# Kernel tuning notes

Hardware: AMD Instinct MI355X
Metric: run time of the kernel (lower is better)

Reference implementation:

```python
import jax, jax.numpy as jnp
import numpy as np

DEPTH = 3
HIDDEN = 300
ATOM_FDIM = 133
BOND_FDIM = 147


def setup_inputs() -> dict:
    key = jax.random.key(0)
    ks = jax.random.split(key, 10)
    n_atoms, n_bonds, max_nb, n_mols = 200000, 400000, 6, 10000
    f_atoms = jax.random.normal(ks[0], (n_atoms, ATOM_FDIM), dtype=jnp.float32)
    f_bonds = jax.random.normal(ks[1], (n_bonds, BOND_FDIM), dtype=jnp.float32)
    a2b = jax.random.randint(ks[2], (n_atoms, max_nb), 0, n_bonds)
    b2a = jax.random.randint(ks[3], (n_bonds,), 0, n_atoms)
    b2revb = jax.random.randint(ks[4], (n_bonds,), 0, n_bonds)
    # learned parameters (fan-in scaled)
    W_i = jax.random.normal(ks[5], (BOND_FDIM, HIDDEN), dtype=jnp.float32) / np.sqrt(BOND_FDIM)
    W_h = jax.random.normal(ks[6], (HIDDEN, HIDDEN), dtype=jnp.float32) / np.sqrt(HIDDEN)
    W_o = jax.random.normal(ks[7], (ATOM_FDIM + HIDDEN, HIDDEN), dtype=jnp.float32) / np.sqrt(ATOM_FDIM + HIDDEN)
    b_o = jnp.zeros((HIDDEN,), dtype=jnp.float32)
    return {"f_atoms": f_atoms, "f_bonds": f_bonds, "a2b": a2b, "b2a": b2a,
            "b2revb": b2revb, "W_i": W_i, "W_h": W_h, "W_o": W_o, "b_o": b_o,
            "n_mols": n_mols}


def reference(f_atoms, f_bonds, a2b, b2a, b2revb, W_i, W_h, W_o, b_o, n_mols):
    act = jax.nn.relu
    # input = W_i(f_bonds); message = act(input)
    inp = f_bonds @ W_i                       # [n_bonds, H]
    message = act(inp)
    for _ in range(DEPTH - 1):
        nei_a_message = message[a2b]          # [n_atoms, max_nb, H] gather
        a_message = nei_a_message.sum(axis=1)  # [n_atoms, H]
        rev_message = message[b2revb]         # [n_bonds, H]
        message = a_message[b2a] - rev_message
        message = act(inp + message @ W_h)
    # final atom readout
    a_message = message[a2b].sum(axis=1)      # [n_atoms, H]
    a_input = jnp.concatenate([f_atoms, a_message], axis=1)
    atom_hiddens = act(a_input @ W_o + b_o)   # [n_atoms, H]
    # scope-based mean pooling (uniform molecules: n_atoms = n_mols * apm)
    apm = f_atoms.shape[0] // n_mols
    mol_vecs = atom_hiddens.reshape(n_mols, apm, HIDDEN).mean(axis=1)
    return mol_vecs
```

## Files before the change

kernel.cpp:

```cpp
#include <hip/hip_runtime.h>
#include <hip/hip_bf16.h>
#include <cstdint>
#include <cstddef>

#define HP 320

typedef unsigned short ushortT;
typedef __attribute__((ext_vector_type(8))) __bf16 bf16x8;
typedef __attribute__((ext_vector_type(4))) float f32x4;

__device__ __forceinline__ float b2f(unsigned u) {
    union { unsigned i; float f; } v; v.i = u << 16; return v.f;
}
__device__ __forceinline__ ushortT f2b(float f) {
    union { float f; unsigned i; } v; v.f = f;
    unsigned x = v.i;
    return (ushortT)((x + 0x7fffu + ((x >> 16) & 1u)) >> 16);
}
__device__ __forceinline__ unsigned subpk(unsigned a, unsigned r) {
    union { unsigned i; float f; } al, ah, rl, rh;
    al.i = a << 16; ah.i = a & 0xffff0000u;
    rl.i = r << 16; rh.i = r & 0xffff0000u;
    float lo = al.f - rl.f, hi = ah.f - rh.f;
    return (unsigned)f2b(lo) | ((unsigned)f2b(hi) << 16);
}
__device__ __forceinline__ uint4 subpk4(uint4 a, uint4 r) {
    uint4 o;
    o.x = subpk(a.x, r.x); o.y = subpk(a.y, r.y);
    o.z = subpk(a.z, r.z); o.w = subpk(a.w, r.w);
    return o;
}
__device__ __forceinline__ void upadd(uint4 u, float* s) {
    s[0] += b2f(u.x & 0xffff); s[1] += b2f(u.x >> 16);
    s[2] += b2f(u.y & 0xffff); s[3] += b2f(u.y >> 16);
    s[4] += b2f(u.z & 0xffff); s[5] += b2f(u.z >> 16);
    s[6] += b2f(u.w & 0xffff); s[7] += b2f(u.w >> 16);
}
__device__ __forceinline__ uint4 pk8(const float* s) {
    uint4 o;
    o.x = (unsigned)f2b(s[0]) | ((unsigned)f2b(s[1]) << 16);
    o.y = (unsigned)f2b(s[2]) | ((unsigned)f2b(s[3]) << 16);
    o.z = (unsigned)f2b(s[4]) | ((unsigned)f2b(s[5]) << 16);
    o.w = (unsigned)f2b(s[6]) | ((unsigned)f2b(s[7]) << 16);
    return o;
}

__device__ __forceinline__ void pack_one(int idx, const float* __restrict__ W,
                                         int Ksrc, ushortT* __restrict__ dst) {
    int j = idx & 7, col = (idx >> 3) & 15, kg = (idx >> 7) & 3;
    int t = idx >> 9; int nt = t % 20, kt = t / 20;
    int k = kt * 32 + kg * 8 + j, n = nt * 16 + col;
    float v = (k < Ksrc && n < 300) ? W[k * 300 + n] : 0.f;
    dst[idx] = f2b(v);
}
__device__ __forceinline__ void pack_wo(int idx, const float* __restrict__ W,
                                        ushortT* __restrict__ dst) {
    int j = idx & 7, col = (idx >> 3) & 15, kg = (idx >> 7) & 3;
    int t = idx >> 9; int nt = t % 20, kt = t / 20;
    int k = kt * 32 + kg * 8 + j, n = nt * 16 + col;
    int src = (k < 133) ? k : ((k >= 160 && k < 460) ? (k - 27) : -1);
    float v = (src >= 0 && n < 300) ? W[src * 300 + n] : 0.f;
    dst[idx] = f2b(v);
}

__global__ __launch_bounds__(256) void k_pack_weights(
    const float* __restrict__ Wi, const float* __restrict__ Wh,
    const float* __restrict__ Wo, const float* __restrict__ bo,
    ushortT* __restrict__ Wipk, ushortT* __restrict__ Whpk,
    ushortT* __restrict__ Wopk, float* __restrict__ bop) {
    int idx = blockIdx.x * 256 + threadIdx.x;
    if (idx < 51200)  pack_one(idx, Wi, 147, Wipk);
    if (idx < 102400) pack_one(idx, Wh, 300, Whpk);
    if (idx < 153600) pack_wo(idx, Wo, Wopk);
    if (idx < HP) bop[idx] = (idx < 300) ? bo[idx] : 0.f;
}

template <int MODE, bool AUXP>
__global__ __launch_bounds__(256, 3) void k_mfma(
    const float* __restrict__ fa, const float* __restrict__ fb,
    const ushortT* __restrict__ aux,
    const ushortT* __restrict__ amsg,
    const ushortT* __restrict__ msgin,
    const int* __restrict__ b2a, const int* __restrict__ b2revb,
    const int* __restrict__ a2b,
    const ushortT* __restrict__ Bpk1, const ushortT* __restrict__ Bpk2,
    const float* __restrict__ bop,
    ushortT* __restrict__ outp,
    ushortT* __restrict__ auxw) {
    constexpr int KT = (MODE == 0) ? 5 : 15;
    constexpr int SPLIT = (MODE == 1) ? 10 : KT;
    constexpr int SP = (MODE == 0) ? 168 : ((MODE == 1) ? 328 : 488);
    __shared__ __align__(16) ushortT panel[64 * SP];
    __shared__ int idxA[(MODE == 1) ? 64 : 1];
    __shared__ int idxR[(MODE == 1) ? 64 : 1];
    __shared__ int idx6[(MODE == 2) ? 64 * 6 : 1];

    const int tid = threadIdx.x, wave = tid >> 6, lane = tid & 63;
    const int row0 = blockIdx.x * 64;
    const int kg8 = (lane >> 4) * 8;
    const int l15 = lane & 15;

    if (MODE == 1) {
        if (tid < 64) {
            idxA[tid] = b2a[row0 + tid];
            idxR[tid] = b2revb[row0 + tid];
        }
        __syncthreads();
    } else if (MODE == 2) {
        if (tid < 64) {
            int a = row0 + tid;
#pragma unroll
            for (int j = 0; j < 6; j++) idx6[tid * 6 + j] = a2b[a * 6 + j];
        }
        __syncthreads();
    }

    if (MODE == 1) {
#pragma unroll
        for (int it = 0; it < 10; it++) {
            int flat = tid + 256 * it;
            int row = flat / 40, ch = flat - row * 40;
            size_t oa = (size_t)idxA[row] * HP;
            size_t orv = (size_t)idxR[row] * HP;
            uint4 ua = *(const uint4*)(amsg + oa + ch * 8);
            uint4 ur = *(const uint4*)(msgin + orv + ch * 8);
            *(uint4*)&panel[row * SP + ch * 8] = subpk4(ua, ur);
        }
    } else if (MODE == 0) {
#pragma unroll
        for (int it = 0; it < 5; it++) {
            int flat = tid + 256 * it;
            int row = flat / 20, ch = flat - row * 20;
            union { ushortT u[8]; uint4 w; } t;
#pragma unroll
            for (int j = 0; j < 8; j++) {
                int k = ch * 8 + j;
                t.u[j] = (k < 147) ? f2b(fb[(size_t)(row0 + row) * 147 + k]) : (ushortT)0;
            }
            *(uint4*)&panel[row * SP + ch * 8] = t.w;
            if (AUXP) *(uint4*)(auxw + (size_t)(row0 + row) * 160 + ch * 8) = t.w;
        }
    } else {
#pragma unroll
        for (int it = 0; it < 15; it++) {
            int flat = tid + 256 * it;
            int row = flat / 60, ch = flat - row * 60;
            uint4 v;
            if (ch >= 20) {
                int kc = (ch - 20) * 8;
                float s[8];
#pragma unroll
                for (int e = 0; e < 8; e++) s[e] = 0.f;
#pragma unroll
                for (int j = 0; j < 6; j++) {
                    uint4 u = *(const uint4*)(msgin + (size_t)idx6[row * 6 + j] * HP + kc);
                    upadd(u, s);
                }
                v = pk8(s);
            } else {
                union { ushortT u[8]; uint4 w; } t;
#pragma unroll
                for (int j = 0; j < 8; j++) {
                    int k = ch * 8 + j;
                    t.u[j] = (k < 133) ? f2b(fa[(size_t)(row0 + row) * 133 + k]) : (ushortT)0;
                }
                v = t.w;
            }
            *(uint4*)&panel[row * SP + ch * 8] = v;
        }
    }

    f32x4 acc[4][5];
#pragma unroll
    for (int i = 0; i < 4; i++)
#pragma unroll
        for (int n = 0; n < 5; n++) acc[i][n] = (f32x4){0.f, 0.f, 0.f, 0.f};

    uint4 breg[2][5];
    const int boff = wave * 5 * 512 + (lane >> 4) * 128 + l15 * 8;

#define LOADB(kt, buf)                                                               \
    {                                                                                \
        const ushortT* bp = ((kt) < SPLIT) ? (Bpk1 + (size_t)(kt) * 10240)           \
                                           : (Bpk2 + (size_t)((kt) - SPLIT) * 10240);\
        _Pragma("unroll")                                                            \
        for (int n = 0; n < 5; n++)                                                  \
            breg[buf][n] = *(const uint4*)(bp + boff + n * 512);                     \
    }

#define MSTEP(bufi, pk0)                                                             \
    {                                                                                \
        bf16x8 a0 = *(bf16x8*)&panel[(l15) * SP + (pk0) + kg8];                      \
        bf16x8 a1 = *(bf16x8*)&panel[(16 + l15) * SP + (pk0) + kg8];                 \
        bf16x8 a2 = *(bf16x8*)&panel[(32 + l15) * SP + (pk0) + kg8];                 \
        bf16x8 a3 = *(bf16x8*)&panel[(48 + l15) * SP + (pk0) + kg8];                 \
        __builtin_amdgcn_s_setprio(1);                                               \
        _Pragma("unroll")                                                            \
        for (int n = 0; n < 5; n++) {                                                \
            bf16x8 b;                                                                \
            *(uint4*)&b = breg[bufi][n];                                             \
            acc[0][n] = __builtin_amdgcn_mfma_f32_16x16x32_bf16(b, a0, acc[0][n], 0, 0, 0); \
            acc[1][n] = __builtin_amdgcn_mfma_f32_16x16x32_bf16(b, a1, acc[1][n], 0, 0, 0); \
            acc[2][n] = __builtin_amdgcn_mfma_f32_16x16x32_bf16(b, a2, acc[2][n], 0, 0, 0); \
            acc[3][n] = __builtin_amdgcn_mfma_f32_16x16x32_bf16(b, a3, acc[3][n], 0, 0, 0); \
        }                                                                            \
        __builtin_amdgcn_s_setprio(0);                                               \
    }

    LOADB(0, 0);
    __syncthreads();

    if (MODE == 1) {
#pragma unroll
        for (int kt = 0; kt < 10; kt++) {
            LOADB(kt + 1, (kt + 1) & 1);
            MSTEP(kt & 1, kt * 32);
        }
        __syncthreads();
#pragma unroll
        for (int it = 0; it < 5; it++) {
            int flat = tid + 256 * it;
            int row = flat / 20, ch = flat - row * 20;
            uint4 v;
            if (AUXP) {
                v = *(const uint4*)(aux + (size_t)(row0 + row) * 160 + ch * 8);
            } else {
                union { ushortT u[8]; uint4 w; } t;
#pragma unroll
                for (int j = 0; j < 8; j++) {
                    int k = ch * 8 + j;
                    t.u[j] = (k < 147) ? f2b(fb[(size_t)(row0 + row) * 147 + k]) : (ushortT)0;
                }
                v = t.w;
            }
            *(uint4*)&panel[row * SP + ch * 8] = v;
        }
        __syncthreads();
#pragma unroll
        for (int kt = 10; kt < 15; kt++) {
            if (kt + 1 < 15) LOADB(kt + 1, (kt + 1) & 1);
            MSTEP(kt & 1, (kt - 10) * 32);
        }
    } else {
#pragma unroll
        for (int kt = 0; kt < KT; kt++) {
            if (kt + 1 < KT) LOADB(kt + 1, (kt + 1) & 1);
            MSTEP(kt & 1, kt * 32);
        }
    }
#undef LOADB
#undef MSTEP

#pragma unroll
    for (int i = 0; i < 4; i++) {
        size_t gr = (size_t)(row0 + i * 16 + l15);
#pragma unroll
        for (int n = 0; n < 5; n++) {
            int col = wave * 80 + n * 16 + (lane >> 4) * 4;
            float4 v = make_float4(acc[i][n][0], acc[i][n][1], acc[i][n][2], acc[i][n][3]);
            if (MODE == 2) {
                float4 bias = *(const float4*)&bop[col];
                v.x += bias.x; v.y += bias.y; v.z += bias.z; v.w += bias.w;
            }
            ushort4 u;
            u.x = f2b(fmaxf(v.x, 0.f)); u.y = f2b(fmaxf(v.y, 0.f));
            u.z = f2b(fmaxf(v.z, 0.f)); u.w = f2b(fmaxf(v.w, 0.f));
            *(ushort4*)&outp[gr * HP + col] = u;
        }
    }
}

__global__ __launch_bounds__(256) void k_atom_sum(
    const ushortT* __restrict__ msg, const int* __restrict__ a2b,
    ushortT* __restrict__ amsg, int nA) {
    int t = blockIdx.x * 256 + threadIdx.x;
    int a = t / 40, q = t - a * 40;
    if (a >= nA) return;
    float s[8];
#pragma unroll
    for (int e = 0; e < 8; e++) s[e] = 0.f;
#pragma unroll
    for (int j = 0; j < 6; j++) {
        int b = a2b[a * 6 + j];
        uint4 u = *(const uint4*)(msg + (size_t)b * HP + q * 8);
        upadd(u, s);
    }
    *(uint4*)(amsg + (size_t)a * HP + q * 8) = pk8(s);
}

__global__ __launch_bounds__(256) void k_pool(
    const ushortT* __restrict__ ah, float* __restrict__ out, int n_mols, int apm) {
    int t = blockIdx.x * 256 + threadIdx.x;
    int m = t / 75, c4 = t - m * 75;
    if (m >= n_mols) return;
    float4 s = make_float4(0, 0, 0, 0);
    for (int u = 0; u < apm; u++) {
        ushort4 q = *(const ushort4*)&ah[(size_t)(m * apm + u) * HP + c4 * 4];
        s.x += b2f(q.x); s.y += b2f(q.y); s.z += b2f(q.z); s.w += b2f(q.w);
    }
    float inv = 1.0f / (float)apm;
    s.x *= inv; s.y *= inv; s.z *= inv; s.w *= inv;
    *(float4*)&out[(size_t)m * 300 + c4 * 4] = s;
}

extern "C" void kernel_launch(void* const* d_in, const int* in_sizes, int n_in,
                              void* d_out, int out_size, void* d_ws, size_t ws_size,
                              hipStream_t stream) {
    const float* fa     = (const float*)d_in[0];
    const float* fb     = (const float*)d_in[1];
    const int*   a2b    = (const int*)d_in[2];
    const int*   b2a    = (const int*)d_in[3];
    const int*   b2revb = (const int*)d_in[4];
    const float* Wi     = (const float*)d_in[5];
    const float* Wh     = (const float*)d_in[6];
    const float* Wo     = (const float*)d_in[7];
    const float* bo     = (const float*)d_in[8];

    const int nA     = in_sizes[0] / 133;
    const int nB     = in_sizes[1] / 147;
    const int n_mols = out_size / 300;
    const int apm    = nA / n_mols;

    char* p = (char*)d_ws;
    ushortT* Wipk = (ushortT*)p;  p += (size_t)51200 * 2;
    ushortT* Whpk = (ushortT*)p;  p += (size_t)102400 * 2;
    ushortT* Wopk = (ushortT*)p;  p += (size_t)153600 * 2;
    float*   bop  = (float*)p;    p += (size_t)HP * 4;
    p = (char*)(((uintptr_t)p + 255) & ~(uintptr_t)255);

    const size_t msgBytes  = (size_t)nB * HP * 2;
    const size_t amsgBytes = (size_t)nA * HP * 2;
    const size_t fbbBytes  = (size_t)nB * 160 * 2;
    const size_t headBytes = (size_t)(p - (char*)d_ws);
    const bool use_fbb = ws_size >= headBytes + 2 * msgBytes + amsgBytes + fbbBytes;

    ushortT* msgA = (ushortT*)p;  p += msgBytes;
    ushortT* msgB = (ushortT*)p;  p += msgBytes;
    ushortT* amsg = (ushortT*)p;  p += amsgBytes;
    ushortT* fbb  = use_fbb ? (ushortT*)p : nullptr;
    ushortT* ah   = msgB;
    float*   out  = (float*)d_out;

    k_pack_weights<<<600, 256, 0, stream>>>(Wi, Wh, Wo, bo, Wipk, Whpk, Wopk, bop);

    const int asum_grid = (int)(((size_t)nA * 40 + 255) / 256);
    const int gB = nB / 64, gA = nA / 64;

    if (use_fbb)
        k_mfma<0, true ><<<gB, 256, 0, stream>>>(fa, fb, nullptr, nullptr, nullptr, nullptr, nullptr,
                                                 nullptr, Wipk, Wipk, bop, msgA, fbb);
    else
        k_mfma<0, false><<<gB, 256, 0, stream>>>(fa, fb, nullptr, nullptr, nullptr, nullptr, nullptr,
                                                 nullptr, Wipk, Wipk, bop, msgA, nullptr);

    k_atom_sum<<<asum_grid, 256, 0, stream>>>(msgA, a2b, amsg, nA);
    if (use_fbb)
        k_mfma<1, true ><<<gB, 256, 0, stream>>>(fa, fb, fbb, amsg, msgA, b2a, b2revb, nullptr,
                                                 Whpk, Wipk, bop, msgB, nullptr);
    else
        k_mfma<1, false><<<gB, 256, 0, stream>>>(fa, fb, nullptr, amsg, msgA, b2a, b2revb, nullptr,
                                                 Whpk, Wipk, bop, msgB, nullptr);

    k_atom_sum<<<asum_grid, 256, 0, stream>>>(msgB, a2b, amsg, nA);
    if (use_fbb)
        k_mfma<1, true ><<<gB, 256, 0, stream>>>(fa, fb, fbb, amsg, msgB, b2a, b2revb, nullptr,
                                                 Whpk, Wipk, bop, msgA, nullptr);
    else
        k_mfma<1, false><<<gB, 256, 0, stream>>>(fa, fb, nullptr, amsg, msgB, b2a, b2revb, nullptr,
                                                 Whpk, Wipk, bop, msgA, nullptr);

    k_mfma<2, false><<<gA, 256, 0, stream>>>(fa, fb, nullptr, nullptr, msgA, nullptr, nullptr, a2b,
                                             Wopk, Wopk, bop, ah, nullptr);
    k_pool<<<((n_mols * 75) + 255) / 256, 256, 0, stream>>>(ah, out, n_mols, apm);
}
```

Measured before the change: 1.363 ms.

## Overlap panel gather with MFMA steps and split final atom-sum into separate kernel

Panel fill is now staged: the first K-chunk is built before the MFMA loop, and later chunks are loaded from global memory while earlier chunks run through the MFMA pipeline. This hides gather latency behind matrix math. The final readout's 6-way neighbour sum moves out of the MODE 2 kernel into a separate k_atom_sum launch, so the readout kernel only streams amsg contiguously. That adds a kernel launch and an extra write and read of amsg, and needs more syncs and live registers.

Result: no change. 1.360 ms (-0.2%).

```diff
diff --git a/kernel.cpp b/kernel.cpp
--- a/kernel.cpp
+++ b/kernel.cpp
@@ -82,7 +82,6 @@
     const ushortT* __restrict__ amsg,
     const ushortT* __restrict__ msgin,
     const int* __restrict__ b2a, const int* __restrict__ b2revb,
-    const int* __restrict__ a2b,
     const ushortT* __restrict__ Bpk1, const ushortT* __restrict__ Bpk2,
     const float* __restrict__ bop,
     ushortT* __restrict__ outp,
@@ -93,7 +92,6 @@
     __shared__ __align__(16) ushortT panel[64 * SP];
     __shared__ int idxA[(MODE == 1) ? 64 : 1];
     __shared__ int idxR[(MODE == 1) ? 64 : 1];
-    __shared__ int idx6[(MODE == 2) ? 64 * 6 : 1];
 
     const int tid = threadIdx.x, wave = tid >> 6, lane = tid & 63;
     const int row0 = blockIdx.x * 64;
@@ -106,68 +104,6 @@
             idxR[tid] = b2revb[row0 + tid];
         }
         __syncthreads();
-    } else if (MODE == 2) {
-        if (tid < 64) {
-            int a = row0 + tid;
-#pragma unroll
-            for (int j = 0; j < 6; j++) idx6[tid * 6 + j] = a2b[a * 6 + j];
-        }
-        __syncthreads();
-    }
-
-    if (MODE == 1) {
-#pragma unroll
-        for (int it = 0; it < 10; it++) {
-            int flat = tid + 256 * it;
-            int row = flat / 40, ch = flat - row * 40;
-            size_t oa = (size_t)idxA[row] * HP;
-            size_t orv = (size_t)idxR[row] * HP;
-            uint4 ua = *(const uint4*)(amsg + oa + ch * 8);
-            uint4 ur = *(const uint4*)(msgin + orv + ch * 8);
-            *(uint4*)&panel[row * SP + ch * 8] = subpk4(ua, ur);
-        }
-    } else if (MODE == 0) {
-#pragma unroll
-        for (int it = 0; it < 5; it++) {
-            int flat = tid + 256 * it;
-            int row = flat / 20, ch = flat - row * 20;
-            union { ushortT u[8]; uint4 w; } t;
-#pragma unroll
-            for (int j = 0; j < 8; j++) {
-                int k = ch * 8 + j;
-                t.u[j] = (k < 147) ? f2b(fb[(size_t)(row0 + row) * 147 + k]) : (ushortT)0;
-            }
-            *(uint4*)&panel[row * SP + ch * 8] = t.w;
-            if (AUXP) *(uint4*)(auxw + (size_t)(row0 + row) * 160 + ch * 8) = t.w;
-        }
-    } else {
-#pragma unroll
-        for (int it = 0; it < 15; it++) {
-            int flat = tid + 256 * it;
-            int row = flat / 60, ch = flat - row * 60;
-            uint4 v;
-            if (ch >= 20) {
-                int kc = (ch - 20) * 8;
-                float s[8];
-#pragma unroll
-                for (int e = 0; e < 8; e++) s[e] = 0.f;
-#pragma unroll
-                for (int j = 0; j < 6; j++) {
-                    uint4 u = *(const uint4*)(msgin + (size_t)idx6[row * 6 + j] * HP + kc);
-                    upadd(u, s);
-                }
-                v = pk8(s);
-            } else {
-                union { ushortT u[8]; uint4 w; } t;
-#pragma unroll
-                for (int j = 0; j < 8; j++) {
-                    int k = ch * 8 + j;
-                    t.u[j] = (k < 133) ? f2b(fa[(size_t)(row0 + row) * 133 + k]) : (ushortT)0;
-                }
-                v = t.w;
-            }
-            *(uint4*)&panel[row * SP + ch * 8] = v;
-        }
     }
 
     f32x4 acc[4][5];
@@ -207,33 +143,70 @@
         __builtin_amdgcn_s_setprio(0);                                               \
     }
 
-    LOADB(0, 0);
-    __syncthreads();
-
-    if (MODE == 1) {
-#pragma unroll
-        for (int kt = 0; kt < 10; kt++) {
-            LOADB(kt + 1, (kt + 1) & 1);
-            MSTEP(kt & 1, kt * 32);
-        }
-        __syncthreads();
+#define BUILD_FEAT(src, FD, row, ch, vout)                                           \
+    {                                                                                \
+        union { ushortT u[8]; uint4 w; } t;                                          \
+        _Pragma("unroll")                                                            \
+        for (int j = 0; j < 8; j++) {                                                \
+            int k = (ch) * 8 + j;                                                    \
+            t.u[j] = (k < FD) ? f2b(src[(size_t)(row) * FD + k]) : (ushortT)0;       \
+        }                                                                            \
+        vout = t.w;                                                                  \
+    }
+
+    if (MODE == 0) {
 #pragma unroll
         for (int it = 0; it < 5; it++) {
             int flat = tid + 256 * it;
             int row = flat / 20, ch = flat - row * 20;
             uint4 v;
+            BUILD_FEAT(fb, 147, row0 + row, ch, v);
+            *(uint4*)&panel[row * SP + ch * 8] = v;
+            if (AUXP) *(uint4*)(auxw + (size_t)(row0 + row) * 160 + ch * 8) = v;
+        }
+        LOADB(0, 0);
+        __syncthreads();
+#pragma unroll
+        for (int kt = 0; kt < 5; kt++) {
+            if (kt + 1 < 5) LOADB(kt + 1, (kt + 1) & 1);
+            MSTEP(kt & 1, kt * 32);
+        }
+    } else if (MODE == 1) {
+#pragma unroll
+        for (int it = 0; it < 5; it++) {
+            int flat = tid + 256 * it;
+            int row = flat / 20, ch = flat - row * 20;
+            uint4 ua = *(const uint4*)(amsg + (size_t)idxA[row] * HP + ch * 8);
+            uint4 ur = *(const uint4*)(msgin + (size_t)idxR[row] * HP + ch * 8);
+            *(uint4*)&panel[row * SP + ch * 8] = subpk4(ua, ur);
+        }
+        LOADB(0, 0);
+        __syncthreads();
+#pragma unroll
+        for (int kt = 0; kt < 5; kt++) {
+            LOADB(kt + 1, (kt + 1) & 1);
+            int flat = tid + 256 * kt;
+            int srow = flat / 20, sch = flat - srow * 20;
+            uint4 ua = *(const uint4*)(amsg + (size_t)idxA[srow] * HP + 160 + sch * 8);
+            uint4 ur = *(const uint4*)(msgin + (size_t)idxR[srow] * HP + 160 + sch * 8);
+            MSTEP(kt & 1, kt * 32);
+            *(uint4*)&panel[srow * SP + 160 + sch * 8] = subpk4(ua, ur);
+        }
+        __syncthreads();
+#pragma unroll
+        for (int kt = 5; kt < 10; kt++) {
+            LOADB(kt + 1, (kt + 1) & 1);
+            int flat = tid + 256 * (kt - 5);
+            int srow = flat / 20, sch = flat - srow * 20;
+            uint4 v;
             if (AUXP) {
-                v = *(const uint4*)(aux + (size_t)(row0 + row) * 160 + ch * 8);
+                v = *(const uint4*)(aux + (size_t)(row0 + srow) * 160 + sch * 8);
+                MSTEP(kt & 1, kt * 32);
             } else {
-                union { ushortT u[8]; uint4 w; } t;
-#pragma unroll
-                for (int j = 0; j < 8; j++) {
-                    int k = ch * 8 + j;
-                    t.u[j] = (k < 147) ? f2b(fb[(size_t)(row0 + row) * 147 + k]) : (ushortT)0;
-                }
-                v = t.w;
+                BUILD_FEAT(fb, 147, row0 + srow, sch, v);
+                MSTEP(kt & 1, kt * 32);
             }
-            *(uint4*)&panel[row * SP + ch * 8] = v;
+            *(uint4*)&panel[srow * SP + sch * 8] = v;
         }
         __syncthreads();
 #pragma unroll
@@ -243,13 +216,37 @@
         }
     } else {
 #pragma unroll
-        for (int kt = 0; kt < KT; kt++) {
-            if (kt + 1 < KT) LOADB(kt + 1, (kt + 1) & 1);
+        for (int it = 0; it < 5; it++) {
+            int flat = tid + 256 * it;
+            int row = flat / 20, ch = flat - row * 20;
+            uint4 v;
+            BUILD_FEAT(fa, 133, row0 + row, ch, v);
+            *(uint4*)&panel[row * SP + ch * 8] = v;
+        }
+        LOADB(0, 0);
+        __syncthreads();
+#pragma unroll
+        for (int kt = 0; kt < 5; kt++) {
+            LOADB(kt + 1, (kt + 1) & 1);
+            int f0 = tid + 256 * (2 * kt), f1 = tid + 256 * (2 * kt + 1);
+            int r0 = f0 / 40, c0 = f0 - r0 * 40;
+            int r1 = f1 / 40, c1 = f1 - r1 * 40;
+            uint4 v0 = *(const uint4*)(amsg + (size_t)(row0 + r0) * HP + c0 * 8);
+            uint4 v1 = *(const uint4*)(amsg + (size_t)(row0 + r1) * HP + c1 * 8);
+            MSTEP(kt & 1, kt * 32);
+            *(uint4*)&panel[r0 * SP + 160 + c0 * 8] = v0;
+            *(uint4*)&panel[r1 * SP + 160 + c1 * 8] = v1;
+        }
+        __syncthreads();
+#pragma unroll
+        for (int kt = 5; kt < 15; kt++) {
+            if (kt + 1 < 15) LOADB(kt + 1, (kt + 1) & 1);
             MSTEP(kt & 1, kt * 32);
         }
     }
 #undef LOADB
 #undef MSTEP
+#undef BUILD_FEAT
 
 #pragma unroll
     for (int i = 0; i < 4; i++) {
@@ -348,28 +345,29 @@
 
     if (use_fbb)
         k_mfma<0, true ><<<gB, 256, 0, stream>>>(fa, fb, nullptr, nullptr, nullptr, nullptr, nullptr,
-                                                 nullptr, Wipk, Wipk, bop, msgA, fbb);
+                                                 Wipk, Wipk, bop, msgA, fbb);
     else
         k_mfma<0, false><<<gB, 256, 0, stream>>>(fa, fb, nullptr, nullptr, nullptr, nullptr, nullptr,
-                                                 nullptr, Wipk, Wipk, bop, msgA, nullptr);
+                                                 Wipk, Wipk, bop, msgA, nullptr);
 
     k_atom_sum<<<asum_grid, 256, 0, stream>>>(msgA, a2b, amsg, nA);
     if (use_fbb)
-        k_mfma<1, true ><<<gB, 256, 0, stream>>>(fa, fb, fbb, amsg, msgA, b2a, b2revb, nullptr,
+        k_mfma<1, true ><<<gB, 256, 0, stream>>>(fa, fb, fbb, amsg, msgA, b2a, b2revb,
                                                  Whpk, Wipk, bop, msgB, nullptr);
     else
-        k_mfma<1, false><<<gB, 256, 0, stream>>>(fa, fb, nullptr, amsg, msgA, b2a, b2revb, nullptr,
+        k_mfma<1, false><<<gB, 256, 0, stream>>>(fa, fb, nullptr, amsg, msgA, b2a, b2revb,
                                                  Whpk, Wipk, bop, msgB, nullptr);
 
     k_atom_sum<<<asum_grid, 256, 0, stream>>>(msgB, a2b, amsg, nA);
     if (use_fbb)
-        k_mfma<1, true ><<<gB, 256, 0, stream>>>(fa, fb, fbb, amsg, msgB, b2a, b2revb, nullptr,
+        k_mfma<1, true ><<<gB, 256, 0, stream>>>(fa, fb, fbb, amsg, msgB, b2a, b2revb,
                                                  Whpk, Wipk, bop, msgA, nullptr);
     else
-        k_mfma<1, false><<<gB, 256, 0, stream>>>(fa, fb, nullptr, amsg, msgB, b2a, b2revb, nullptr,
+        k_mfma<1, false><<<gB, 256, 0, stream>>>(fa, fb, nullptr, amsg, msgB, b2a, b2revb,
                                                  Whpk, Wipk, bop, msgA, nullptr);
 
-    k_mfma<2, false><<<gA, 256, 0, stream>>>(fa, fb, nullptr, nullptr, msgA, nullptr, nullptr, a2b,
+    k_atom_sum<<<asum_grid, 256, 0, stream>>>(msgA, a2b, amsg, nA);
+    k_mfma<2, false><<<gA, 256, 0, stream>>>(fa, fb, nullptr, amsg, nullptr, nullptr, nullptr,
                                              Wopk, Wopk, bop, ah, nullptr);
     k_pool<<<((n_mols * 75) + 255) / 256, 256, 0, stream>>>(ah, out, n_mols, apm);
 }
```
